# Performance work log

Hardware: AMD Instinct MI355X
Metric: run time of the kernel (lower is better)

The kernel has to match this reference:

```python
import jax, jax.numpy as jnp
import numpy as np

QLEN, B, D, NH, DH, DI = 1024, 4, 1024, 16, 64, 4096
KLEN = QLEN
RLEN = QLEN + KLEN
EPS = 1e-12
SCALE = 1.0 / (DH ** 0.5)


def layer_norm(x, g, b):
    mu = jnp.mean(x, axis=-1, keepdims=True)
    var = jnp.mean(jnp.square(x - mu), axis=-1, keepdims=True)
    return (x - mu) * jax.lax.rsqrt(var + EPS) * g + b


def rel_shift(x, klen):
    # x: [qlen, rlen, b, n] -> [qlen, klen, b, n] via XLNet reshape trick
    q, r_, b, n = x.shape
    x = jnp.reshape(x, (r_, q, b, n))[1:]
    x = jnp.reshape(x, (q, r_ - 1, b, n))[:, :klen]
    return x


def setup_inputs() -> dict:
    key = jax.random.key(0)
    ks = jax.random.split(key, 16)
    std = 0.02
    h = jax.random.normal(ks[0], (QLEN, B, D), jnp.float32)
    r = jax.random.normal(ks[1], (RLEN, B, D), jnp.float32)
    # causal mask: 1 where key position j > query position i (disallowed)
    m = (jnp.arange(KLEN)[None, :] > jnp.arange(QLEN)[:, None]).astype(jnp.float32)
    attn_mask = jnp.broadcast_to(m[:, :, None, None], (QLEN, KLEN, B, 1))
    # segment matrix: one-hot of (seg_i != seg_j), shape [q, k, b, 2]
    seg_ids = jax.random.randint(ks[2], (QLEN, B), 0, 2)
    diff = (seg_ids[:, None, :] != seg_ids[None, :, :]).astype(jnp.int32)
    seg_mat = jax.nn.one_hot(diff, 2, dtype=jnp.float32)
    p = lambda k, shape: jax.random.normal(k, shape, jnp.float32) * std
    return {
        'h': h, 'r': r, 'attn_mask': attn_mask, 'seg_mat': seg_mat,
        'q_w': p(ks[3], (D, NH, DH)), 'k_w': p(ks[4], (D, NH, DH)),
        'v_w': p(ks[5], (D, NH, DH)), 'o_w': p(ks[6], (D, NH, DH)),
        'r_w': p(ks[7], (D, NH, DH)),
        'r_r_bias': jnp.zeros((NH, DH), jnp.float32),
        'r_s_bias': jnp.zeros((NH, DH), jnp.float32),
        'r_w_bias': jnp.zeros((NH, DH), jnp.float32),
        'seg_embed': p(ks[8], (2, NH, DH)),
        'ln1_g': jnp.ones((D,), jnp.float32), 'ln1_b': jnp.zeros((D,), jnp.float32),
        'ff_w1': p(ks[9], (D, DI)), 'ff_b1': jnp.zeros((DI,), jnp.float32),
        'ff_w2': p(ks[10], (DI, D)), 'ff_b2': jnp.zeros((D,), jnp.float32),
        'ln2_g': jnp.ones((D,), jnp.float32), 'ln2_b': jnp.zeros((D,), jnp.float32),
    }


def reference(h, r, attn_mask, seg_mat, q_w, k_w, v_w, o_w, r_w,
              r_r_bias, r_s_bias, r_w_bias, seg_embed,
              ln1_g, ln1_b, ff_w1, ff_b1, ff_w2, ff_b2, ln2_g, ln2_b):
    # projections (single-stream: g=None, mems=None => cat == h)
    q_head = jnp.einsum('ibh,hnd->ibnd', h, q_w)
    k_head = jnp.einsum('ibh,hnd->ibnd', h, k_w)
    v_head = jnp.einsum('ibh,hnd->ibnd', h, v_w)
    k_r = jnp.einsum('ibh,hnd->ibnd', r, r_w)
    # content + relative position + segment bias terms
    ac = jnp.einsum('ibnd,jbnd->ijbn', q_head + r_w_bias, k_head)
    bd = jnp.einsum('ibnd,jbnd->ijbn', q_head + r_r_bias, k_r)
    bd = rel_shift(bd, KLEN)
    ef = jnp.einsum('ibnd,snd->ibns', q_head + r_s_bias, seg_embed)
    ef = jnp.einsum('ijbs,ibns->ijbn', seg_mat, ef)
    attn_score = (ac + bd + ef) * SCALE - 1e30 * attn_mask
    attn_prob = jax.nn.softmax(attn_score, axis=1)
    attn_vec = jnp.einsum('ijbn,jbnd->ibnd', attn_prob, v_head)
    # post-attention
    attn_out = jnp.einsum('ibnd,hnd->ibh', attn_vec, o_w) + h
    out = layer_norm(attn_out, ln1_g, ln1_b)
    # feed-forward
    ff = jax.nn.gelu(jnp.einsum('ibh,hf->ibf', out, ff_w1) + ff_b1, approximate=False)
    ff = jnp.einsum('ibf,fh->ibh', ff, ff_w2) + ff_b2
    return layer_norm(ff + out, ln2_g, ln2_b)
```

## Files before the change

### kernel.cpp

```cpp
#include <hip/hip_runtime.h>
#include <hip/hip_bf16.h>

using bf16 = __hip_bfloat16;
typedef __attribute__((ext_vector_type(8))) short short8;
typedef __attribute__((ext_vector_type(4))) float floatx4;

#define QLEN 1024
#define KLEN 1024
#define RLEN 2048
#define RUSED 1152
#define BB   4
#define DMODEL 1024
#define NH   16
#define DH   64
#define DI   4096
#define ND   1024
#define QKVS 3072
#define SCALE 0.125f

__device__ inline void gl_lds16(const bf16* g, bf16* l) {
  __builtin_amdgcn_global_load_lds(
      (__attribute__((address_space(1))) void*)(g),
      (__attribute__((address_space(3))) void*)(l), 16, 0, 0);
}

__global__ __launch_bounds__(256) void cvt_all(
    const float* __restrict__ h, const float* __restrict__ r,
    const float* __restrict__ ow,
    bf16* __restrict__ hb, bf16* __restrict__ rb, bf16* __restrict__ wo)
{
  const int id = blockIdx.x;
  const float* src; bf16* dst; int off;
  if (id < 2048)      { src = h;  dst = hb; off = id * 2048; }
  else if (id < 4352) { src = r;  dst = rb; off = (id - 2048) * 2048; }
  else                { src = ow; dst = wo; off = (id - 4352) * 2048; }
  const int idx = off + threadIdx.x * 8;
  const float4 a = *reinterpret_cast<const float4*>(src + idx);
  const float4 b = *reinterpret_cast<const float4*>(src + idx + 4);
  bf16 o[8] = {__float2bfloat16(a.x), __float2bfloat16(a.y),
               __float2bfloat16(a.z), __float2bfloat16(a.w),
               __float2bfloat16(b.x), __float2bfloat16(b.y),
               __float2bfloat16(b.z), __float2bfloat16(b.w)};
  *reinterpret_cast<uint4*>(dst + idx) = *reinterpret_cast<uint4*>(o);
}

__device__ inline void tconv_tile(const float* __restrict__ src, bf16* __restrict__ dst,
                                  int R, int C, int bx, int by, int tid) {
  __shared__ float tile[32][33];
  const int r0 = by * 32, c0 = bx * 32;
  {
    const int tr = tid >> 3, tc = (tid & 7) * 4;
    const float4 f = *reinterpret_cast<const float4*>(src + (size_t)(r0 + tr) * C + c0 + tc);
    tile[tr][tc + 0] = f.x; tile[tr][tc + 1] = f.y;
    tile[tr][tc + 2] = f.z; tile[tr][tc + 3] = f.w;
  }
  __syncthreads();
  {
    const int oc = tid >> 3, orr = (tid & 7) * 4;
    bf16 o[4];
#pragma unroll
    for (int u = 0; u < 4; ++u) o[u] = __float2bfloat16(tile[orr + u][oc]);
    *reinterpret_cast<uint2*>(dst + (size_t)(c0 + oc) * R + r0 + orr) = *reinterpret_cast<uint2*>(o);
  }
}

__global__ __launch_bounds__(256) void tconv_all(
    const float* __restrict__ qw, const float* __restrict__ kw,
    const float* __restrict__ vw, const float* __restrict__ rw,
    const float* __restrict__ w1, const float* __restrict__ w2,
    bf16* __restrict__ wqkvt, bf16* __restrict__ wrt,
    bf16* __restrict__ w1t, bf16* __restrict__ w2t)
{
  const int id = blockIdx.x;
  const int tid = threadIdx.x;
  if (id < 4096) {
    const int part = id >> 10, local = id & 1023;
    const float* src = (part == 0) ? qw : (part == 1) ? kw : (part == 2) ? vw : rw;
    bf16* dst = (part < 3) ? (wqkvt + (size_t)part * ND * DMODEL) : wrt;
    tconv_tile(src, dst, DMODEL, ND, local & 31, local >> 5, tid);
  } else if (id < 8192) {
    const int local = id - 4096;
    tconv_tile(w1, w1t, DMODEL, DI, local & 127, local >> 7, tid);
  } else {
    const int local = id - 8192;
    tconv_tile(w2, w2t, DI, DMODEL, local & 31, local >> 5, tid);
  }
}

__global__ __launch_bounds__(256) void seg_extract(const float* __restrict__ seg,
                                                   float* __restrict__ dsb) {
  const int idx = blockIdx.x * 256 + threadIdx.x;
  const int i = idx >> 2, b = idx & 3;
  dsb[b * QLEN + i] = seg[(size_t)(i * KLEN * BB + b) * 2 + 1];
}

__global__ __launch_bounds__(256) void gemm_bt(
    const bf16* __restrict__ A, const bf16* __restrict__ Bt,
    int M, int N, int K, int Ktot, int lda, int ldb,
    const float* __restrict__ bias, const float* __restrict__ resid, int act_gelu,
    float* __restrict__ outf, bf16* __restrict__ outb, int pstride)
{
  __shared__ bf16 As[128][32];
  __shared__ bf16 Bs[128][32];

  const int tid = threadIdx.x;
  const int m0b = blockIdx.y * 128;
  const int n0b = blockIdx.x * 128;
  const int z = blockIdx.z;
  const int kbeg = z * K;
  const int kcnt = min(K, Ktot - kbeg);
  A  += (size_t)kbeg;
  Bt += (size_t)kbeg;
  float* of = outf ? (outf + (size_t)z * pstride) : outf;
  bf16*  ob = outb ? (outb + (size_t)z * pstride) : outb;

  const int wave = tid >> 6, lane = tid & 63;
  const int wm = (wave & 1) * 64, wn = (wave >> 1) * 64;
  const int fl = lane & 15, quad = lane >> 4;

  const int lr = lane >> 2;
  const int cg = (((lane & 3) ^ ((lr >> 1) & 3)) << 3);
  const bf16* ga0 = A  + (size_t)(m0b + wave * 32 + lr) * lda + cg;
  const bf16* ga1 = ga0 + (size_t)16 * lda;
  const bf16* gb0 = Bt + (size_t)(n0b + wave * 32 + lr) * ldb + cg;
  const bf16* gb1 = gb0 + (size_t)16 * ldb;
  bf16* la0 = &As[wave * 32 + lr][(lane & 3) * 8];
  bf16* la1 = &As[wave * 32 + 16 + lr][(lane & 3) * 8];
  bf16* lb0 = &Bs[wave * 32 + lr][(lane & 3) * 8];
  bf16* lb1 = &Bs[wave * 32 + 16 + lr][(lane & 3) * 8];

  const int rc = ((quad ^ ((fl >> 1) & 3)) << 3);

  floatx4 acc[4][4];
#pragma unroll
  for (int mi = 0; mi < 4; ++mi)
#pragma unroll
    for (int ni = 0; ni < 4; ++ni) acc[mi][ni] = (floatx4){0.f, 0.f, 0.f, 0.f};

  for (int k0 = 0; k0 < kcnt; k0 += 32) {
    __syncthreads();
    gl_lds16(ga0 + k0, la0);
    gl_lds16(ga1 + k0, la1);
    gl_lds16(gb0 + k0, lb0);
    gl_lds16(gb1 + k0, lb1);
    __syncthreads();

    short8 af[4], bfv[4];
#pragma unroll
    for (int mi = 0; mi < 4; ++mi)
      af[mi] = *reinterpret_cast<const short8*>(&As[wm + mi * 16 + fl][rc]);
#pragma unroll
    for (int ni = 0; ni < 4; ++ni)
      bfv[ni] = *reinterpret_cast<const short8*>(&Bs[wn + ni * 16 + fl][rc]);
#pragma unroll
    for (int mi = 0; mi < 4; ++mi)
#pragma unroll
      for (int ni = 0; ni < 4; ++ni)
        acc[mi][ni] = __builtin_amdgcn_mfma_f32_16x16x32_bf16(af[mi], bfv[ni], acc[mi][ni], 0, 0, 0);
  }

#pragma unroll
  for (int mi = 0; mi < 4; ++mi) {
#pragma unroll
    for (int r = 0; r < 4; ++r) {
      const int row = m0b + wm + mi * 16 + quad * 4 + r;
#pragma unroll
      for (int ni = 0; ni < 4; ++ni) {
        const int col = n0b + wn + ni * 16 + fl;
        float v = acc[mi][ni][r];
        if (bias) v += bias[col];
        if (act_gelu) v = 0.5f * v * (1.0f + erff(v * 0.70710678118654752f));
        const size_t base = (size_t)row * N + col;
        if (resid) v += resid[base];
        if (of) of[base] = v;
        if (ob) ob[base] = __float2bfloat16(v);
      }
    }
  }
}

__global__ __launch_bounds__(512, 4) void gemm256(
    const bf16* __restrict__ A, const bf16* __restrict__ Bt,
    int M, int N, int K, int Ktot, int lda, int ldb,
    const float* __restrict__ bias, int act_gelu,
    bf16* __restrict__ outb, int pstride)
{
  __shared__ __attribute__((aligned(16))) bf16 As[2][128 * 64];
  __shared__ __attribute__((aligned(16))) bf16 Bs[2][128 * 64];

  const int tid = threadIdx.x;
  const int wave = tid >> 6, lane = tid & 63;

  const int gX = gridDim.x;
  const int nwg = gX * gridDim.y;
  int lin = blockIdx.y * gX + blockIdx.x;
  {
    const int q = nwg >> 3, r = nwg & 7;
    const int xcd = lin & 7, idx = lin >> 3;
    lin = (xcd < r ? xcd * (q + 1) : r * (q + 1) + (xcd - r) * q) + idx;
  }
  const int n0b = (lin % gX) << 7;
  const int m0b = (lin / gX) << 7;

  const int z = blockIdx.z;
  const int kbeg = z * K;
  const int nkt = min(K, Ktot - kbeg) >> 6;
  const bf16* Ab = A + (size_t)kbeg;
  const bf16* Bb = Bt + (size_t)kbeg;
  bf16* ob = outb + (size_t)z * pstride;

  const int srow = lane >> 3;
  const int scol = ((lane & 7) ^ srow) << 3;
  const bf16* gA = Ab + (size_t)(m0b + wave * 8 + srow) * lda + scol;
  const bf16* gB = Bb + (size_t)(n0b + wave * 8 + srow) * ldb + scol;
  const int lofs = wave * (8 * 64) + lane * 8;
  bf16* lA[2] = {&As[0][lofs], &As[1][lofs]};
  bf16* lB[2] = {&Bs[0][lofs], &Bs[1][lofs]};

  const int fl = lane & 15, quad = lane >> 4;
  const int wm = (wave >> 2) * 64;
  const int wn = (wave & 3) * 32;
  const int ch0 = (quad ^ (fl & 7)) << 3;

  floatx4 acc[4][2];
#pragma unroll
  for (int mi = 0; mi < 4; ++mi)
#pragma unroll
    for (int ni = 0; ni < 2; ++ni) acc[mi][ni] = (floatx4){0.f, 0.f, 0.f, 0.f};

  {
    gl_lds16(gA, lA[0]);
    gl_lds16(gA + (size_t)64 * lda, lA[0] + 4096);
    gl_lds16(gB, lB[0]);
    gl_lds16(gB + (size_t)64 * ldb, lB[0] + 4096);
  }
  if (nkt > 1) {
    gl_lds16(gA + 64, lA[1]);
    gl_lds16(gA + (size_t)64 * lda + 64, lA[1] + 4096);
    gl_lds16(gB + 64, lB[1]);
    gl_lds16(gB + (size_t)64 * ldb + 64, lB[1] + 4096);
  }

  for (int kt = 0; kt < nkt; ++kt) {
    if (kt + 1 < nkt) {
      asm volatile("s_waitcnt vmcnt(4)" ::: "memory");
    } else {
      asm volatile("s_waitcnt vmcnt(0)" ::: "memory");
    }
    __builtin_amdgcn_s_barrier();
    __builtin_amdgcn_sched_barrier(0);

    const bf16* as = (kt & 1) ? &As[1][0] : &As[0][0];
    const bf16* bs = (kt & 1) ? &Bs[1][0] : &Bs[0][0];
#pragma unroll
    for (int ks = 0; ks < 2; ++ks) {
      const int ch = ch0 ^ (ks << 5);
      short8 af[4], bv[2];
#pragma unroll
      for (int mi = 0; mi < 4; ++mi)
        af[mi] = *reinterpret_cast<const short8*>(&as[(wm + mi * 16 + fl) * 64 + ch]);
#pragma unroll
      for (int ni = 0; ni < 2; ++ni)
        bv[ni] = *reinterpret_cast<const short8*>(&bs[(wn + ni * 16 + fl) * 64 + ch]);
      __builtin_amdgcn_s_setprio(1);
#pragma unroll
      for (int mi = 0; mi < 4; ++mi)
#pragma unroll
        for (int ni = 0; ni < 2; ++ni)
          acc[mi][ni] = __builtin_amdgcn_mfma_f32_16x16x32_bf16(af[mi], bv[ni], acc[mi][ni], 0, 0, 0);
      __builtin_amdgcn_s_setprio(0);
    }
    __builtin_amdgcn_sched_barrier(0);
    __builtin_amdgcn_s_barrier();
    if (kt + 2 < nkt) {
      const size_t ko = (size_t)(kt + 2) << 6;
      bf16* dA = (kt & 1) ? lA[1] : lA[0];
      bf16* dB = (kt & 1) ? lB[1] : lB[0];
      gl_lds16(gA + ko, dA);
      gl_lds16(gA + (size_t)64 * lda + ko, dA + 4096);
      gl_lds16(gB + ko, dB);
      gl_lds16(gB + (size_t)64 * ldb + ko, dB + 4096);
    }
  }

#pragma unroll
  for (int mi = 0; mi < 4; ++mi) {
#pragma unroll
    for (int r = 0; r < 4; ++r) {
      const int row = m0b + wm + mi * 16 + quad * 4 + r;
#pragma unroll
      for (int ni = 0; ni < 2; ++ni) {
        const int col = n0b + wn + ni * 16 + fl;
        float v = acc[mi][ni][r];
        if (bias) v += bias[col];
        if (act_gelu) v = 0.5f * v * (1.0f + erff(v * 0.70710678118654752f));
        ob[(size_t)row * N + col] = __float2bfloat16(v);
      }
    }
  }
}

__global__ __launch_bounds__(256, 3) void attn_kernel(
    const bf16* __restrict__ qkv, const bf16* __restrict__ kr,
    const float* __restrict__ dsb, const float* __restrict__ seg_embed,
    const float* __restrict__ rwb, const float* __restrict__ rrb,
    const float* __restrict__ rsb,
    bf16* __restrict__ av_out)
{
  const int bx = blockIdx.x;
  const int n  = bx & 15;
  const int b  = (bx >> 4) & 3;
  const int it = 15 - (bx >> 6);
  const int i0 = it * 64;
  const int tid = threadIdx.x;

  const bf16* qh = qkv + n * DH;
  const bf16* kh = qkv + ND + n * DH;
  const bf16* vh = qkv + 2 * ND + n * DH;

  __shared__ bf16 Kb[64][72];
  __shared__ bf16 VT[64][72];
  __shared__ bf16 krw[128][72];
  __shared__ bf16 bdrL[64][88];
  __shared__ float efs0[64], efs1[64];
  __shared__ float dsq[64], dsk[64];

  const int wave = tid >> 6, lane = tid & 63;
  const int fl = lane & 15, quad = lane >> 4;
  const int wq0 = wave * 16;
  const int tb0 = 3 - wave;
  const int twoc = (tid & 3) << 1;

  short8 aw[2], ar[2];
  {
    const int qrow = i0 + wq0 + fl;
    const bf16* qp = qh + (size_t)(qrow * BB + b) * QKVS;
    float e0 = 0.f, e1 = 0.f;
#pragma unroll
    for (int ks = 0; ks < 2; ++ks) {
      const int d0 = ks * 32 + quad * 8;
      const uint4 qv = *reinterpret_cast<const uint4*>(qp + d0);
      const bf16* qe = reinterpret_cast<const bf16*>(&qv);
      bf16 wt[8], rt[8];
#pragma unroll
      for (int u = 0; u < 8; ++u) {
        const int d = d0 + u;
        const float qf = __bfloat162float(qe[u]);
        wt[u] = __float2bfloat16(qf + rwb[n * DH + d]);
        rt[u] = __float2bfloat16(qf + rrb[n * DH + d]);
        const float qs = qf + rsb[n * DH + d];
        e0 += qs * seg_embed[(0 * NH + n) * DH + d];
        e1 += qs * seg_embed[(1 * NH + n) * DH + d];
      }
      aw[ks] = *reinterpret_cast<short8*>(wt);
      ar[ks] = *reinterpret_cast<short8*>(rt);
    }
    e0 += __shfl_xor(e0, 16, 64); e0 += __shfl_xor(e0, 32, 64);
    e1 += __shfl_xor(e1, 16, 64); e1 += __shfl_xor(e1, 32, 64);
    if (quad == 0) { efs0[wq0 + fl] = e0; efs1[wq0 + fl] = e1; }
    if (tid < 64) dsq[tid] = dsb[b * QLEN + i0 + tid];
  }

  floatx4 O[4];
#pragma unroll
  for (int nb = 0; nb < 4; ++nb) O[nb] = (floatx4){0.f, 0.f, 0.f, 0.f};
  float l_loc[4] = {0.f, 0.f, 0.f, 0.f};

  for (int jt = 0; jt <= it; ++jt) {
    const int j0 = jt * 64;
    const int kbase = QLEN + j0 - i0 - 63;

    __syncthreads();

    {
      const int j  = tid >> 2;
      const int dc = (tid & 3) << 4;
      const bf16* kp = kh + (size_t)((j0 + j) * BB + b) * QKVS + dc;
      const uint4 k0v = reinterpret_cast<const uint4*>(kp)[0];
      const uint4 k1v = reinterpret_cast<const uint4*>(kp)[1];
      reinterpret_cast<uint4*>(&Kb[j][dc])[0] = k0v;
      reinterpret_cast<uint4*>(&Kb[j][dc + 8])[0] = k1v;
      const bf16* vp = vh + (size_t)((j0 + j) * BB + b) * QKVS + dc;
      const uint4 v0v = reinterpret_cast<const uint4*>(vp)[0];
      const uint4 v1v = reinterpret_cast<const uint4*>(vp)[1];
      const bf16* ve0 = reinterpret_cast<const bf16*>(&v0v);
      const bf16* ve1 = reinterpret_cast<const bf16*>(&v1v);
#pragma unroll
      for (int u = 0; u < 8; ++u) {
        VT[dc + (u ^ twoc)][j] = ve0[u];
        VT[dc + 8 + (u ^ twoc)][j] = ve1[u];
      }
      const int t   = tid >> 1;
      const int dc2 = (tid & 1) << 5;
      const bf16* rp = kr + ((size_t)((kbase + t) * BB + b)) * ND + n * DH + dc2;
#pragma unroll
      for (int u = 0; u < 4; ++u)
        reinterpret_cast<uint4*>(&krw[t][dc2 + u * 8])[0] = reinterpret_cast<const uint4*>(rp)[u];
      if (tid < 64) dsk[tid] = dsb[b * QLEN + j0 + tid];
    }
    __syncthreads();

    floatx4 accS[4], accB[5];
#pragma unroll
    for (int nb = 0; nb < 4; ++nb) accS[nb] = (floatx4){0.f, 0.f, 0.f, 0.f};
#pragma unroll
    for (int u = 0; u < 5; ++u) accB[u] = (floatx4){0.f, 0.f, 0.f, 0.f};
#pragma unroll
    for (int ks = 0; ks < 2; ++ks) {
#pragma unroll
      for (int nb = 0; nb < 4; ++nb)
        accS[nb] = __builtin_amdgcn_mfma_f32_16x16x32_bf16(
            aw[ks], *reinterpret_cast<const short8*>(&Kb[nb * 16 + fl][ks * 32 + quad * 8]), accS[nb], 0, 0, 0);
#pragma unroll
      for (int u = 0; u < 5; ++u)
        accB[u] = __builtin_amdgcn_mfma_f32_16x16x32_bf16(
            ar[ks], *reinterpret_cast<const short8*>(&krw[(tb0 + u) * 16 + fl][ks * 32 + quad * 8]), accB[u], 0, 0, 0);
    }
#pragma unroll
    for (int u = 0; u < 5; ++u)
#pragma unroll
      for (int r = 0; r < 4; ++r)
        bdrL[wq0 + quad * 4 + r][u * 16 + fl] = __float2bfloat16(accB[u][r]);

    float pv[4][4];
#pragma unroll
    for (int r = 0; r < 4; ++r) {
      const int qL = wq0 + quad * 4 + r;
      const int qg = i0 + qL;
      const float e0q = efs0[qL], e1q = efs1[qL];
      const float dq = dsq[qL];
#pragma unroll
      for (int nb = 0; nb < 4; ++nb) {
        const int kL = nb * 16 + fl;
        const int kg = j0 + kL;
        const float bdv = __bfloat162float(bdrL[qL][15 + kL - quad * 4 - r]);
        const float ef = (dq != dsk[kL]) ? e1q : e0q;
        const float s = (accS[nb][r] + bdv + ef) * SCALE;
        const float pe = (kg > qg) ? 0.0f : __expf(s);
        pv[nb][r] = pe;
        l_loc[r] += pe;
      }
    }

#pragma unroll
    for (int nb = 0; nb < 4; ++nb)
#pragma unroll
      for (int r = 0; r < 4; ++r)
        bdrL[wq0 + quad * 4 + r][nb * 16 + fl] = __float2bfloat16(pv[nb][r]);

#pragma unroll
    for (int ks = 0; ks < 2; ++ks) {
      const short8 ap = *reinterpret_cast<const short8*>(&bdrL[wq0 + fl][ks * 32 + quad * 8]);
#pragma unroll
      for (int nb = 0; nb < 4; ++nb)
        O[nb] = __builtin_amdgcn_mfma_f32_16x16x32_bf16(
            ap, *reinterpret_cast<const short8*>(&VT[nb * 16 + (fl ^ (nb << 1))][ks * 32 + quad * 8]), O[nb], 0, 0, 0);
    }
  }

  float inv[4];
#pragma unroll
  for (int r = 0; r < 4; ++r) {
    float l = l_loc[r];
    l += __shfl_xor(l, 1, 64);
    l += __shfl_xor(l, 2, 64);
    l += __shfl_xor(l, 4, 64);
    l += __shfl_xor(l, 8, 64);
    inv[r] = 1.0f / l;
  }
#pragma unroll
  for (int r = 0; r < 4; ++r) {
    const int qL = wq0 + quad * 4 + r;
    bf16* op = av_out + ((size_t)((i0 + qL) * BB + b)) * ND + n * DH;
#pragma unroll
    for (int nb = 0; nb < 4; ++nb)
      op[nb * 16 + fl] = __float2bfloat16(O[nb][r] * inv[r]);
  }
}

__global__ __launch_bounds__(256) void ln_fused(
    const float* __restrict__ pa, const float* __restrict__ pb,
    const float* __restrict__ resid,
    const float* __restrict__ gg, const float* __restrict__ bbias,
    float* __restrict__ outf, bf16* __restrict__ outb)
{
  const int row = blockIdx.x;
  const int tid = threadIdx.x;
  __shared__ float red[4];
  const size_t base = (size_t)row * DMODEL;

  float v[4];
  float s = 0.0f;
#pragma unroll
  for (int k = 0; k < 4; ++k) {
    const int c = k * 256 + tid;
    const float x = pa[base + c] + pb[base + c] + resid[base + c];
    v[k] = x;
    s += x;
  }
#pragma unroll
  for (int off = 32; off; off >>= 1) s += __shfl_xor(s, off, 64);
  const int w = tid >> 6, lane = tid & 63;
  if (lane == 0) red[w] = s;
  __syncthreads();
  const float mean = (red[0] + red[1] + red[2] + red[3]) * (1.0f / DMODEL);

  float s2 = 0.0f;
#pragma unroll
  for (int k = 0; k < 4; ++k) {
    const float dlt = v[k] - mean;
    s2 += dlt * dlt;
  }
  __syncthreads();
#pragma unroll
  for (int off = 32; off; off >>= 1) s2 += __shfl_xor(s2, off, 64);
  if (lane == 0) red[w] = s2;
  __syncthreads();
  const float var = (red[0] + red[1] + red[2] + red[3]) * (1.0f / DMODEL);
  const float rstd = rsqrtf(var + 1e-12f);

#pragma unroll
  for (int k = 0; k < 4; ++k) {
    const int c = k * 256 + tid;
    const float o = (v[k] - mean) * rstd * gg[c] + bbias[c];
    if (outf) outf[base + c] = o;
    if (outb) outb[base + c] = __float2bfloat16(o);
  }
}

__global__ __launch_bounds__(256) void ln_fused4b(
    const bf16* __restrict__ pa, const bf16* __restrict__ pb,
    const bf16* __restrict__ pc, const bf16* __restrict__ pd,
    const float* __restrict__ resid, const float* __restrict__ bias,
    const float* __restrict__ gg, const float* __restrict__ bbias,
    float* __restrict__ outf)
{
  const int row = blockIdx.x;
  const int tid = threadIdx.x;
  __shared__ float red[4];
  const size_t base = (size_t)row * DMODEL;

  float v[4];
  float s = 0.0f;
#pragma unroll
  for (int k = 0; k < 4; ++k) {
    const int c = k * 256 + tid;
    float x = __bfloat162float(pa[base + c]) + __bfloat162float(pb[base + c]) +
              __bfloat162float(pc[base + c]) + __bfloat162float(pd[base + c]) +
              resid[base + c] + bias[c];
    v[k] = x;
    s += x;
  }
#pragma unroll
  for (int off = 32; off; off >>= 1) s += __shfl_xor(s, off, 64);
  const int w = tid >> 6, lane = tid & 63;
  if (lane == 0) red[w] = s;
  __syncthreads();
  const float mean = (red[0] + red[1] + red[2] + red[3]) * (1.0f / DMODEL);

  float s2 = 0.0f;
#pragma unroll
  for (int k = 0; k < 4; ++k) {
    const float dlt = v[k] - mean;
    s2 += dlt * dlt;
  }
  __syncthreads();
#pragma unroll
  for (int off = 32; off; off >>= 1) s2 += __shfl_xor(s2, off, 64);
  if (lane == 0) red[w] = s2;
  __syncthreads();
  const float var = (red[0] + red[1] + red[2] + red[3]) * (1.0f / DMODEL);
  const float rstd = rsqrtf(var + 1e-12f);

#pragma unroll
  for (int k = 0; k < 4; ++k) {
    const int c = k * 256 + tid;
    outf[base + c] = (v[k] - mean) * rstd * gg[c] + bbias[c];
  }
}

extern "C" void kernel_launch(void* const* d_in, const int* in_sizes, int n_in,
                              void* d_out, int out_size, void* d_ws, size_t ws_size,
                              hipStream_t stream) {
  const float* h         = (const float*)d_in[0];
  const float* r         = (const float*)d_in[1];
  const float* seg_mat   = (const float*)d_in[3];
  const float* q_w       = (const float*)d_in[4];
  const float* k_w       = (const float*)d_in[5];
  const float* v_w       = (const float*)d_in[6];
  const float* o_w       = (const float*)d_in[7];
  const float* r_w       = (const float*)d_in[8];
  const float* r_r_bias  = (const float*)d_in[9];
  const float* r_s_bias  = (const float*)d_in[10];
  const float* r_w_bias  = (const float*)d_in[11];
  const float* seg_embed = (const float*)d_in[12];
  const float* ln1_g     = (const float*)d_in[13];
  const float* ln1_b     = (const float*)d_in[14];
  const float* ff_w1     = (const float*)d_in[15];
  const float* ff_b1     = (const float*)d_in[16];
  const float* ff_w2     = (const float*)d_in[17];
  const float* ff_b2     = (const float*)d_in[18];
  const float* ln2_g     = (const float*)d_in[19];
  const float* ln2_b     = (const float*)d_in[20];
  float* outp = (float*)d_out;

  const size_t M1 = (size_t)QLEN * BB;
  const size_t MRU = (size_t)RUSED * BB;
  char* ws = (char*)d_ws;
  const size_t MB = 1u << 20;

  bf16* hb   = (bf16*)(ws + 0 * MB);
  bf16* rb   = (bf16*)(ws + 8 * MB);
  bf16* wqkvt= (bf16*)(ws + 24 * MB);
  bf16* wrt  = (bf16*)(ws + 30 * MB);
  bf16* wo   = (bf16*)(ws + 32 * MB);
  bf16* w1t  = (bf16*)(ws + 34 * MB);
  bf16* w2t  = (bf16*)(ws + 42 * MB);
  bf16* qkvb = (bf16*)(ws + 50 * MB);
  bf16* krb  = (bf16*)(ws + 74 * MB);
  bf16* avb  = (bf16*)(ws + 90 * MB);
  float* pa1  = (float*)(ws + 0 * MB);
  float* pb1  = (float*)(ws + 16 * MB);
  float* out1 = (float*)(ws + 50 * MB);
  bf16* out1b = (bf16*)(ws + 66 * MB);
  bf16* ff1   = (bf16*)(ws + 0 * MB);
  bf16* p2    = (bf16*)(ws + 74 * MB);
  float* dsbuf = (float*)(ws + 106 * MB);

  dim3 blk(256);
  dim3 blk512(512);

  cvt_all<<<dim3(4864), blk, 0, stream>>>(h, r, o_w, hb, rb, wo);
  tconv_all<<<dim3(12288), blk, 0, stream>>>(q_w, k_w, v_w, r_w, ff_w1, ff_w2,
                                             wqkvt, wrt, w1t, w2t);
  seg_extract<<<dim3(16), blk, 0, stream>>>(seg_mat, dsbuf);

  gemm256<<<dim3(QKVS / 128, M1 / 128, 1), blk512, 0, stream>>>(
      hb, wqkvt, (int)M1, QKVS, DMODEL, DMODEL, DMODEL, DMODEL, nullptr, 0, qkvb, 0);
  gemm_bt<<<dim3(ND / 128, (int)(MRU / 128), 1), blk, 0, stream>>>(
      rb, wrt, (int)MRU, ND, DMODEL, DMODEL, DMODEL, DMODEL, nullptr, nullptr, 0, nullptr, krb, 0);

  attn_kernel<<<dim3(16 * BB * NH), blk, 0, stream>>>(
      qkvb, krb, dsbuf, seg_embed,
      r_w_bias, r_r_bias, r_s_bias, avb);

  gemm_bt<<<dim3(DMODEL / 128, M1 / 128, 2), blk, 0, stream>>>(
      avb, wo, (int)M1, DMODEL, ND / 2, ND, ND, ND, nullptr, nullptr, 0, pa1, nullptr, (int)(M1 * DMODEL));

  ln_fused<<<dim3((int)M1), blk, 0, stream>>>(pa1, pb1, h, ln1_g, ln1_b, out1, out1b);

  gemm256<<<dim3(DI / 128, M1 / 128, 1), blk512, 0, stream>>>(
      out1b, w1t, (int)M1, DI, DMODEL, DMODEL, DMODEL, DMODEL, ff_b1, 1, ff1, 0);

  gemm256<<<dim3(DMODEL / 128, M1 / 128, 4), blk512, 0, stream>>>(
      ff1, w2t, (int)M1, DMODEL, DI / 4, DI, DI, DI, nullptr, 0, p2, (int)(M1 * DMODEL));

  ln_fused4b<<<dim3((int)M1), blk, 0, stream>>>(
      p2, p2 + M1 * DMODEL, p2 + 2 * M1 * DMODEL, p2 + 3 * M1 * DMODEL,
      out1, ff_b2, ln2_g, ln2_b, outp);
}
```

Before: 466.2 us.

## Replace gemm_bt with gemm256, prefetch attention tiles in registers, halve FF2 split-K

Removes the older 128x128 single-buffered gemm_bt kernel and routes the r-projection and output-projection GEMMs through the double-buffered gemm256 kernel, which now has an optional fp32 output. The attention kernel prefetches the next K/V/kr tile into registers while the current tile is being processed, which hides global-load latency at the cost of more registers. The FF2 GEMM drops from split-K 4 to 2, so the final layernorm reads two bf16 partials instead of four. That halves partial-sum traffic but gives the GEMM fewer workgroups.

New measurement: 432.0 us. 1.08x faster.

```diff
diff --git a/kernel.cpp b/kernel.cpp
--- a/kernel.cpp
+++ b/kernel.cpp
@@ -94,96 +94,11 @@
   dsb[b * QLEN + i] = seg[(size_t)(i * KLEN * BB + b) * 2 + 1];
 }
 
-__global__ __launch_bounds__(256) void gemm_bt(
-    const bf16* __restrict__ A, const bf16* __restrict__ Bt,
-    int M, int N, int K, int Ktot, int lda, int ldb,
-    const float* __restrict__ bias, const float* __restrict__ resid, int act_gelu,
-    float* __restrict__ outf, bf16* __restrict__ outb, int pstride)
-{
-  __shared__ bf16 As[128][32];
-  __shared__ bf16 Bs[128][32];
-
-  const int tid = threadIdx.x;
-  const int m0b = blockIdx.y * 128;
-  const int n0b = blockIdx.x * 128;
-  const int z = blockIdx.z;
-  const int kbeg = z * K;
-  const int kcnt = min(K, Ktot - kbeg);
-  A  += (size_t)kbeg;
-  Bt += (size_t)kbeg;
-  float* of = outf ? (outf + (size_t)z * pstride) : outf;
-  bf16*  ob = outb ? (outb + (size_t)z * pstride) : outb;
-
-  const int wave = tid >> 6, lane = tid & 63;
-  const int wm = (wave & 1) * 64, wn = (wave >> 1) * 64;
-  const int fl = lane & 15, quad = lane >> 4;
-
-  const int lr = lane >> 2;
-  const int cg = (((lane & 3) ^ ((lr >> 1) & 3)) << 3);
-  const bf16* ga0 = A  + (size_t)(m0b + wave * 32 + lr) * lda + cg;
-  const bf16* ga1 = ga0 + (size_t)16 * lda;
-  const bf16* gb0 = Bt + (size_t)(n0b + wave * 32 + lr) * ldb + cg;
-  const bf16* gb1 = gb0 + (size_t)16 * ldb;
-  bf16* la0 = &As[wave * 32 + lr][(lane & 3) * 8];
-  bf16* la1 = &As[wave * 32 + 16 + lr][(lane & 3) * 8];
-  bf16* lb0 = &Bs[wave * 32 + lr][(lane & 3) * 8];
-  bf16* lb1 = &Bs[wave * 32 + 16 + lr][(lane & 3) * 8];
-
-  const int rc = ((quad ^ ((fl >> 1) & 3)) << 3);
-
-  floatx4 acc[4][4];
-#pragma unroll
-  for (int mi = 0; mi < 4; ++mi)
-#pragma unroll
-    for (int ni = 0; ni < 4; ++ni) acc[mi][ni] = (floatx4){0.f, 0.f, 0.f, 0.f};
-
-  for (int k0 = 0; k0 < kcnt; k0 += 32) {
-    __syncthreads();
-    gl_lds16(ga0 + k0, la0);
-    gl_lds16(ga1 + k0, la1);
-    gl_lds16(gb0 + k0, lb0);
-    gl_lds16(gb1 + k0, lb1);
-    __syncthreads();
-
-    short8 af[4], bfv[4];
-#pragma unroll
-    for (int mi = 0; mi < 4; ++mi)
-      af[mi] = *reinterpret_cast<const short8*>(&As[wm + mi * 16 + fl][rc]);
-#pragma unroll
-    for (int ni = 0; ni < 4; ++ni)
-      bfv[ni] = *reinterpret_cast<const short8*>(&Bs[wn + ni * 16 + fl][rc]);
-#pragma unroll
-    for (int mi = 0; mi < 4; ++mi)
-#pragma unroll
-      for (int ni = 0; ni < 4; ++ni)
-        acc[mi][ni] = __builtin_amdgcn_mfma_f32_16x16x32_bf16(af[mi], bfv[ni], acc[mi][ni], 0, 0, 0);
-  }
-
-#pragma unroll
-  for (int mi = 0; mi < 4; ++mi) {
-#pragma unroll
-    for (int r = 0; r < 4; ++r) {
-      const int row = m0b + wm + mi * 16 + quad * 4 + r;
-#pragma unroll
-      for (int ni = 0; ni < 4; ++ni) {
-        const int col = n0b + wn + ni * 16 + fl;
-        float v = acc[mi][ni][r];
-        if (bias) v += bias[col];
-        if (act_gelu) v = 0.5f * v * (1.0f + erff(v * 0.70710678118654752f));
-        const size_t base = (size_t)row * N + col;
-        if (resid) v += resid[base];
-        if (of) of[base] = v;
-        if (ob) ob[base] = __float2bfloat16(v);
-      }
-    }
-  }
-}
-
 __global__ __launch_bounds__(512, 4) void gemm256(
     const bf16* __restrict__ A, const bf16* __restrict__ Bt,
     int M, int N, int K, int Ktot, int lda, int ldb,
     const float* __restrict__ bias, int act_gelu,
-    bf16* __restrict__ outb, int pstride)
+    float* __restrict__ outf, bf16* __restrict__ outb, int pstride)
 {
   __shared__ __attribute__((aligned(16))) bf16 As[2][128 * 64];
   __shared__ __attribute__((aligned(16))) bf16 Bs[2][128 * 64];
@@ -207,7 +122,8 @@
   const int nkt = min(K, Ktot - kbeg) >> 6;
   const bf16* Ab = A + (size_t)kbeg;
   const bf16* Bb = Bt + (size_t)kbeg;
-  bf16* ob = outb + (size_t)z * pstride;
+  float* of = outf ? (outf + (size_t)z * pstride) : outf;
+  bf16*  ob = outb ? (outb + (size_t)z * pstride) : outb;
 
   const int srow = lane >> 3;
   const int scol = ((lane & 7) ^ srow) << 3;
@@ -294,7 +210,9 @@
         float v = acc[mi][ni][r];
         if (bias) v += bias[col];
         if (act_gelu) v = 0.5f * v * (1.0f + erff(v * 0.70710678118654752f));
-        ob[(size_t)row * N + col] = __float2bfloat16(v);
+        const size_t idx = (size_t)row * N + col;
+        if (of) of[idx] = v;
+        else    ob[idx] = __float2bfloat16(v);
       }
     }
   }
@@ -366,38 +284,64 @@
   for (int nb = 0; nb < 4; ++nb) O[nb] = (floatx4){0.f, 0.f, 0.f, 0.f};
   float l_loc[4] = {0.f, 0.f, 0.f, 0.f};
 
+  const int sj  = tid >> 2;
+  const int sdc = (tid & 3) << 4;
+  const int st  = tid >> 1;
+  const int sdc2= (tid & 1) << 5;
+  uint4 kv0, kv1, vv0, vv1, rr0, rr1, rr2, rr3;
+  {
+    const bf16* kp = kh + (size_t)((0 + sj) * BB + b) * QKVS + sdc;
+    kv0 = reinterpret_cast<const uint4*>(kp)[0];
+    kv1 = reinterpret_cast<const uint4*>(kp)[1];
+    const bf16* vp = vh + (size_t)((0 + sj) * BB + b) * QKVS + sdc;
+    vv0 = reinterpret_cast<const uint4*>(vp)[0];
+    vv1 = reinterpret_cast<const uint4*>(vp)[1];
+    const int kbase0 = QLEN - i0 - 63;
+    const bf16* rp = kr + ((size_t)((kbase0 + st) * BB + b)) * ND + n * DH + sdc2;
+    rr0 = reinterpret_cast<const uint4*>(rp)[0];
+    rr1 = reinterpret_cast<const uint4*>(rp)[1];
+    rr2 = reinterpret_cast<const uint4*>(rp)[2];
+    rr3 = reinterpret_cast<const uint4*>(rp)[3];
+  }
+
   for (int jt = 0; jt <= it; ++jt) {
     const int j0 = jt * 64;
-    const int kbase = QLEN + j0 - i0 - 63;
 
     __syncthreads();
 
     {
-      const int j  = tid >> 2;
-      const int dc = (tid & 3) << 4;
-      const bf16* kp = kh + (size_t)((j0 + j) * BB + b) * QKVS + dc;
-      const uint4 k0v = reinterpret_cast<const uint4*>(kp)[0];
-      const uint4 k1v = reinterpret_cast<const uint4*>(kp)[1];
-      reinterpret_cast<uint4*>(&Kb[j][dc])[0] = k0v;
-      reinterpret_cast<uint4*>(&Kb[j][dc + 8])[0] = k1v;
-      const bf16* vp = vh + (size_t)((j0 + j) * BB + b) * QKVS + dc;
-      const uint4 v0v = reinterpret_cast<const uint4*>(vp)[0];
-      const uint4 v1v = reinterpret_cast<const uint4*>(vp)[1];
-      const bf16* ve0 = reinterpret_cast<const bf16*>(&v0v);
-      const bf16* ve1 = reinterpret_cast<const bf16*>(&v1v);
+      reinterpret_cast<uint4*>(&Kb[sj][sdc])[0] = kv0;
+      reinterpret_cast<uint4*>(&Kb[sj][sdc + 8])[0] = kv1;
+      const bf16* ve0 = reinterpret_cast<const bf16*>(&vv0);
+      const bf16* ve1 = reinterpret_cast<const bf16*>(&vv1);
 #pragma unroll
       for (int u = 0; u < 8; ++u) {
-        VT[dc + (u ^ twoc)][j] = ve0[u];
-        VT[dc + 8 + (u ^ twoc)][j] = ve1[u];
+        VT[sdc + (u ^ twoc)][sj] = ve0[u];
+        VT[sdc + 8 + (u ^ twoc)][sj] = ve1[u];
       }
-      const int t   = tid >> 1;
-      const int dc2 = (tid & 1) << 5;
-      const bf16* rp = kr + ((size_t)((kbase + t) * BB + b)) * ND + n * DH + dc2;
-#pragma unroll
-      for (int u = 0; u < 4; ++u)
-        reinterpret_cast<uint4*>(&krw[t][dc2 + u * 8])[0] = reinterpret_cast<const uint4*>(rp)[u];
+      reinterpret_cast<uint4*>(&krw[st][sdc2 + 0])[0]  = rr0;
+      reinterpret_cast<uint4*>(&krw[st][sdc2 + 8])[0]  = rr1;
+      reinterpret_cast<uint4*>(&krw[st][sdc2 + 16])[0] = rr2;
+      reinterpret_cast<uint4*>(&krw[st][sdc2 + 24])[0] = rr3;
       if (tid < 64) dsk[tid] = dsb[b * QLEN + j0 + tid];
     }
+
+    if (jt < it) {
+      const int j0n = j0 + 64;
+      const bf16* kp = kh + (size_t)((j0n + sj) * BB + b) * QKVS + sdc;
+      kv0 = reinterpret_cast<const uint4*>(kp)[0];
+      kv1 = reinterpret_cast<const uint4*>(kp)[1];
+      const bf16* vp = vh + (size_t)((j0n + sj) * BB + b) * QKVS + sdc;
+      vv0 = reinterpret_cast<const uint4*>(vp)[0];
+      vv1 = reinterpret_cast<const uint4*>(vp)[1];
+      const int kbn = QLEN + j0n - i0 - 63;
+      const bf16* rp = kr + ((size_t)((kbn + st) * BB + b)) * ND + n * DH + sdc2;
+      rr0 = reinterpret_cast<const uint4*>(rp)[0];
+      rr1 = reinterpret_cast<const uint4*>(rp)[1];
+      rr2 = reinterpret_cast<const uint4*>(rp)[2];
+      rr3 = reinterpret_cast<const uint4*>(rp)[3];
+    }
+
     __syncthreads();
 
     floatx4 accS[4], accB[5];
@@ -528,9 +472,8 @@
   }
 }
 
-__global__ __launch_bounds__(256) void ln_fused4b(
+__global__ __launch_bounds__(256) void ln_fused2b(
     const bf16* __restrict__ pa, const bf16* __restrict__ pb,
-    const bf16* __restrict__ pc, const bf16* __restrict__ pd,
     const float* __restrict__ resid, const float* __restrict__ bias,
     const float* __restrict__ gg, const float* __restrict__ bbias,
     float* __restrict__ outf)
@@ -546,7 +489,6 @@
   for (int k = 0; k < 4; ++k) {
     const int c = k * 256 + tid;
     float x = __bfloat162float(pa[base + c]) + __bfloat162float(pb[base + c]) +
-              __bfloat162float(pc[base + c]) + __bfloat162float(pd[base + c]) +
               resid[base + c] + bias[c];
     v[k] = x;
     s += x;
@@ -636,26 +578,26 @@
   seg_extract<<<dim3(16), blk, 0, stream>>>(seg_mat, dsbuf);
 
   gemm256<<<dim3(QKVS / 128, M1 / 128, 1), blk512, 0, stream>>>(
-      hb, wqkvt, (int)M1, QKVS, DMODEL, DMODEL, DMODEL, DMODEL, nullptr, 0, qkvb, 0);
-  gemm_bt<<<dim3(ND / 128, (int)(MRU / 128), 1), blk, 0, stream>>>(
-      rb, wrt, (int)MRU, ND, DMODEL, DMODEL, DMODEL, DMODEL, nullptr, nullptr, 0, nullptr, krb, 0);
+      hb, wqkvt, (int)M1, QKVS, DMODEL, DMODEL, DMODEL, DMODEL, nullptr, 0, nullptr, qkvb, 0);
+  gemm256<<<dim3(ND / 128, (int)(MRU / 128), 1), blk512, 0, stream>>>(
+      rb, wrt, (int)MRU, ND, DMODEL, DMODEL, DMODEL, DMODEL, nullptr, 0, nullptr, krb, 0);
 
   attn_kernel<<<dim3(16 * BB * NH), blk, 0, stream>>>(
       qkvb, krb, dsbuf, seg_embed,
       r_w_bias, r_r_bias, r_s_bias, avb);
 
-  gemm_bt<<<dim3(DMODEL / 128, M1 / 128, 2), blk, 0, stream>>>(
-      avb, wo, (int)M1, DMODEL, ND / 2, ND, ND, ND, nullptr, nullptr, 0, pa1, nullptr, (int)(M1 * DMODEL));
+  gemm256<<<dim3(DMODEL / 128, M1 / 128, 2), blk512, 0, stream>>>(
+      avb, wo, (int)M1, DMODEL, ND / 2, ND, ND, ND, nullptr, 0, pa1, nullptr, (int)(M1 * DMODEL));
 
   ln_fused<<<dim3((int)M1), blk, 0, stream>>>(pa1, pb1, h, ln1_g, ln1_b, out1, out1b);
 
   gemm256<<<dim3(DI / 128, M1 / 128, 1), blk512, 0, stream>>>(
-      out1b, w1t, (int)M1, DI, DMODEL, DMODEL, DMODEL, DMODEL, ff_b1, 1, ff1, 0);
-
-  gemm256<<<dim3(DMODEL / 128, M1 / 128, 4), blk512, 0, stream>>>(
-      ff1, w2t, (int)M1, DMODEL, DI / 4, DI, DI, DI, nullptr, 0, p2, (int)(M1 * DMODEL));
-
-  ln_fused4b<<<dim3((int)M1), blk, 0, stream>>>(
-      p2, p2 + M1 * DMODEL, p2 + 2 * M1 * DMODEL, p2 + 3 * M1 * DMODEL,
+      out1b, w1t, (int)M1, DI, DMODEL, DMODEL, DMODEL, DMODEL, ff_b1, 1, nullptr, ff1, 0);
+
+  gemm256<<<dim3(DMODEL / 128, M1 / 128, 2), blk512, 0, stream>>>(
+      ff1, w2t, (int)M1, DMODEL, DI / 2, DI, DI, DI, nullptr, 0, nullptr, p2, (int)(M1 * DMODEL));
+
+  ln_fused2b<<<dim3((int)M1), blk, 0, stream>>>(
+      p2, p2 + M1 * DMODEL,
       out1, ff_b2, ln2_g, ln2_b, outp);
 }
```
